# Kernel optimization log

Hardware: AMD Instinct MI355X
Metric: run time of the kernel (lower is better)

## Reference

```python
import jax, jax.numpy as jnp
import numpy as np

EMBED_DIM = 1024
NUM_HEADS = 16
HEAD_DIM = EMBED_DIM // NUM_HEADS
BATCH = 2
SEQ = 2048


def setup_inputs() -> dict:
    key = jax.random.key(0)
    ks = jax.random.split(key, 9)
    s = EMBED_DIM ** -0.5
    inp = {"x": jax.random.normal(ks[0], (BATCH, SEQ, EMBED_DIM), dtype=jnp.float32)}
    names = ["Wq", "Wk", "Wv", "Wo"]
    for i, n in enumerate(names):
        inp[n] = jax.random.normal(ks[1 + i], (EMBED_DIM, EMBED_DIM), dtype=jnp.float32) * s
        inp["b" + n[1]] = jax.random.normal(ks[5 + i], (EMBED_DIM,), dtype=jnp.float32) * 0.02
    return inp


def reference(x, Wq, bq, Wk, bk, Wv, bv, Wo, bo):
    B, S, E = x.shape
    H, D = NUM_HEADS, HEAD_DIM
    scaling = D ** -0.5
    # projections (torch Linear: x @ W.T + b), reshape to (B, H, S, D)
    q = (x @ Wq.T + bq).reshape(B, S, H, D).transpose(0, 2, 1, 3)
    k = (x @ Wk.T + bk).reshape(B, S, H, D).transpose(0, 2, 1, 3)
    v = (x @ Wv.T + bv).reshape(B, S, H, D).transpose(0, 2, 1, 3)
    # full materialized score matrix, matching the original module
    scores = jnp.einsum("bhqd,bhkd->bhqk", q, k) * scaling
    causal = jnp.triu(jnp.ones((S, S), dtype=bool), k=1)  # True above diagonal
    scores = jnp.where(causal[None, None], -jnp.inf, scores)
    attn = jax.nn.softmax(scores, axis=-1)
    out = jnp.einsum("bhqk,bhkd->bhqd", attn, v)  # (B, H, S, D)
    out = out.transpose(0, 2, 1, 3).reshape(B, S, E)
    return out @ Wo.T + bo
```

## Files before the change

kernel.cpp:

```cpp
#include <hip/hip_runtime.h>
#include <stdint.h>

typedef __bf16 bf16;
typedef __bf16 bf16x8 __attribute__((ext_vector_type(8)));
typedef __bf16 bf16x4 __attribute__((ext_vector_type(4)));
typedef float  f32x4  __attribute__((ext_vector_type(4)));

#define E_DIM 1024
#define S_LEN 2048
#define BATCH 2
#define NH 16
#define DH 64

#define NEG_INF (-__builtin_inff())

__device__ __forceinline__ void load_lds16(const bf16* g, bf16* l) {
    __builtin_amdgcn_global_load_lds(
        (const __attribute__((address_space(1))) void*)g,
        (__attribute__((address_space(3))) void*)l, 16, 0, 0);
}

__global__ __launch_bounds__(256) void convert_kernel(
    const float* __restrict__ s0, const float* __restrict__ s1,
    const float* __restrict__ s2, const float* __restrict__ s3,
    const float* __restrict__ s4,
    bf16* __restrict__ d0, bf16* __restrict__ d1, bf16* __restrict__ d2,
    bf16* __restrict__ d3, bf16* __restrict__ d4,
    int n0, int n1)
{
    const float* src; bf16* dst; int n;
    switch (blockIdx.y) {
        case 0:  src = s0; dst = d0; n = n0; break;
        case 1:  src = s1; dst = d1; n = n1; break;
        case 2:  src = s2; dst = d2; n = n1; break;
        case 3:  src = s3; dst = d3; n = n1; break;
        default: src = s4; dst = d4; n = n1; break;
    }
    int i = (blockIdx.x * 256 + threadIdx.x) * 4;
    if (i >= n) return;
    float4 v = *(const float4*)(src + i);
    bf16x4 o;
    o[0] = (bf16)v.x; o[1] = (bf16)v.y; o[2] = (bf16)v.z; o[3] = (bf16)v.w;
    *(bf16x4*)(dst + i) = o;
}

__global__ __launch_bounds__(256) void gemm_kernel(
    const bf16* __restrict__ A,
    const bf16* __restrict__ W0, const bf16* __restrict__ W1, const bf16* __restrict__ W2,
    const float* __restrict__ bias0, const float* __restrict__ bias1, const float* __restrict__ bias2,
    bf16* __restrict__ outQ, bf16* __restrict__ outK, bf16* __restrict__ outVt,
    float* __restrict__ outF, int final_mode)
{
    __shared__ bf16 As[128 * 32];
    __shared__ bf16 Bs[128 * 32];

    int mode;
    const bf16* W; const float* bias;
    if (final_mode) { mode = 3; W = W0; bias = bias0; }
    else {
        mode = blockIdx.z;
        W    = (mode == 0) ? W0 : (mode == 1 ? W1 : W2);
        bias = (mode == 0) ? bias0 : (mode == 1 ? bias1 : bias2);
    }

    const int bm = blockIdx.y * 128, bn = blockIdx.x * 128;
    const int t = threadIdx.x;
    const int lane = t & 63, w = t >> 6;
    const int quad = lane >> 4, l16 = lane & 15;
    const int wm = (w & 1) * 64, wn = (w >> 1) * 64;

    const int r0 = w * 16;
    const int srow = r0 + (lane >> 2), scol = (lane & 3) * 8;
    const bf16* Ag0 = A + (size_t)(bm + srow) * E_DIM + scol;
    const bf16* Ag1 = Ag0 + (size_t)64 * E_DIM;
    const bf16* Wg0 = W + (size_t)(bn + srow) * E_DIM + scol;
    const bf16* Wg1 = Wg0 + (size_t)64 * E_DIM;
    bf16* lda0 = As + r0 * 32;
    bf16* lda1 = As + (64 + r0) * 32;
    bf16* ldb0 = Bs + r0 * 32;
    bf16* ldb1 = Bs + (64 + r0) * 32;

    f32x4 acc[4][4];
#pragma unroll
    for (int i = 0; i < 4; i++)
#pragma unroll
        for (int j = 0; j < 4; j++) acc[i][j] = f32x4{0.f, 0.f, 0.f, 0.f};

    for (int kt = 0; kt < E_DIM; kt += 32) {
        __syncthreads();
        load_lds16(Ag0 + kt, lda0);
        load_lds16(Ag1 + kt, lda1);
        load_lds16(Wg0 + kt, ldb0);
        load_lds16(Wg1 + kt, ldb1);
        __syncthreads();

        bf16x8 af[4], bfr[4];
#pragma unroll
        for (int i = 0; i < 4; i++)
            af[i] = *(const bf16x8*)(As + (wm + i * 16 + l16) * 32 + quad * 8);
#pragma unroll
        for (int j = 0; j < 4; j++)
            bfr[j] = *(const bf16x8*)(Bs + (wn + j * 16 + l16) * 32 + quad * 8);
#pragma unroll
        for (int i = 0; i < 4; i++)
#pragma unroll
            for (int j = 0; j < 4; j++)
                acc[i][j] = __builtin_amdgcn_mfma_f32_16x16x32_bf16(af[i], bfr[j], acc[i][j], 0, 0, 0);
    }

#pragma unroll
    for (int j = 0; j < 4; j++) {
        const int n = bn + wn + j * 16 + l16;
        const float bv = bias[n];
#pragma unroll
        for (int i = 0; i < 4; i++) {
            const int m0 = bm + wm + i * 16 + quad * 4;
            if (mode == 3) {
#pragma unroll
                for (int r = 0; r < 4; r++)
                    outF[(size_t)(m0 + r) * E_DIM + n] = acc[i][j][r] + bv;
            } else if (mode == 2) {
                const int b_ = m0 >> 11, s0 = m0 & (S_LEN - 1);
                const int h = n >> 6, d = n & 63;
                bf16x4 pv;
#pragma unroll
                for (int r = 0; r < 4; r++) pv[r] = (bf16)(acc[i][j][r] + bv);
                *(bf16x4*)(outVt + ((size_t)((b_ * NH + h) * DH + d)) * S_LEN + s0) = pv;
            } else {
                bf16* o = (mode == 0) ? outQ : outK;
                const float sc = (mode == 0) ? 0.125f : 1.0f;
                const int h = n >> 6, d = n & 63;
#pragma unroll
                for (int r = 0; r < 4; r++) {
                    const int m = m0 + r;
                    const int b_ = m >> 11, s = m & (S_LEN - 1);
                    o[((size_t)(b_ * NH + h) * S_LEN + s) * DH + d] = (bf16)((acc[i][j][r] + bv) * sc);
                }
            }
        }
    }
}

__global__ __launch_bounds__(256, 1) void attn_kernel(
    const bf16* __restrict__ Qb, const bf16* __restrict__ Kb,
    const bf16* __restrict__ Vtb, bf16* __restrict__ Ob)
{
    __shared__ bf16 Ks[128 * 72];
    __shared__ bf16 Vs[64 * 136];
    __shared__ bf16 Ps[4][16 * 136];

    const int t = threadIdx.x, lane = t & 63, w = t >> 6;
    const int quad = lane >> 4, l16 = lane & 15;

    const int i = blockIdx.x;
    const int xcd = i & 7, rr = i >> 3;
    const int bh = (xcd << 2) | (rr & 3);
    const int pr = rr >> 2;
    const int qlo = pr, qhi = 15 - pr;

    const bf16* Qg = Qb + (size_t)bh * S_LEN * DH;
    const bf16* Kg = Kb + (size_t)bh * S_LEN * DH;
    const bf16* Vg = Vtb + (size_t)bh * DH * S_LEN;
    const int b_ = bh >> 4, h = bh & 15;
    bf16* Og = Ob + (size_t)b_ * S_LEN * E_DIM + h * DH;

    bf16* Pw = Ps[w];
    const int inrow0 = w * 32;

    bf16x8 aq[2][2][2];
#pragma unroll
    for (int qt = 0; qt < 2; qt++) {
        const int qrow0 = (qt ? qhi : qlo) * 128 + inrow0;
#pragma unroll
        for (int st = 0; st < 2; st++) {
            const bf16* qp = Qg + (size_t)(qrow0 + st * 16 + l16) * DH + quad * 8;
            aq[qt][st][0] = *(const bf16x8*)(qp);
            aq[qt][st][1] = *(const bf16x8*)(qp + 32);
        }
    }

    f32x4 o[2][2][4];
    float l_part[2][2][4];
#pragma unroll
    for (int qt = 0; qt < 2; qt++)
#pragma unroll
        for (int st = 0; st < 2; st++)
#pragma unroll
            for (int dt = 0; dt < 4; dt++) {
                o[qt][st][dt] = f32x4{0.f, 0.f, 0.f, 0.f};
                l_part[qt][st][dt] = 0.f;
            }

    const int T = qhi + 1;
    const int krow = t >> 3, kcol8 = (t & 7) * 8;
    const int vrow = t >> 4, vcol8 = (t & 15) * 8;

    uint4 kc[4], vc[4];
#pragma unroll
    for (int k = 0; k < 4; k++)
        kc[k] = *(const uint4*)(Kg + (size_t)(krow + 32 * k) * DH + kcol8);
#pragma unroll
    for (int k = 0; k < 4; k++)
        vc[k] = *(const uint4*)(Vg + (size_t)(vrow + 16 * k) * S_LEN + vcol8);

    for (int kt = 0; kt < T; kt++) {
        __syncthreads();
#pragma unroll
        for (int k = 0; k < 4; k++)
            *(uint4*)(Ks + (krow + 32 * k) * 72 + kcol8) = kc[k];
#pragma unroll
        for (int k = 0; k < 4; k++)
            *(uint4*)(Vs + (vrow + 16 * k) * 136 + vcol8) = vc[k];
        __syncthreads();

        if (kt + 1 < T) {
            const int nb = (kt + 1) * 128;
#pragma unroll
            for (int k = 0; k < 4; k++)
                kc[k] = *(const uint4*)(Kg + (size_t)(nb + krow + 32 * k) * DH + kcol8);
#pragma unroll
            for (int k = 0; k < 4; k++)
                vc[k] = *(const uint4*)(Vg + (size_t)(vrow + 16 * k) * S_LEN + nb + vcol8);
        }

#pragma unroll
        for (int qt = 0; qt < 2; qt++) {
            if (qt == 0 && kt > qlo) continue;
            const bool diag = qt ? (kt == qhi) : (kt == qlo);

#pragma unroll
            for (int st = 0; st < 2; st++) {
                const int inrow_base = inrow0 + st * 16 + quad * 4;

                f32x4 sv[8];
#pragma unroll
                for (int jt = 0; jt < 8; jt++) {
                    const bf16* kp = Ks + (jt * 16 + l16) * 72 + quad * 8;
                    bf16x8 bk0 = *(const bf16x8*)(kp);
                    bf16x8 bk1 = *(const bf16x8*)(kp + 32);
                    f32x4 s = f32x4{0.f, 0.f, 0.f, 0.f};
                    s = __builtin_amdgcn_mfma_f32_16x16x32_bf16(aq[qt][st][0], bk0, s, 0, 0, 0);
                    s = __builtin_amdgcn_mfma_f32_16x16x32_bf16(aq[qt][st][1], bk1, s, 0, 0, 0);
                    sv[jt] = s;
                }

                if (diag) {
#pragma unroll
                    for (int jt = 0; jt < 8; jt++) {
                        const int kcol = jt * 16 + l16;
#pragma unroll
                        for (int r = 0; r < 4; r++)
                            if (kcol > inrow_base + r) sv[jt][r] = NEG_INF;
                    }
                }

#pragma unroll
                for (int jt = 0; jt < 8; jt++)
#pragma unroll
                    for (int r = 0; r < 4; r++) {
                        const float pe = __expf(sv[jt][r]);
                        sv[jt][r] = pe;
                        l_part[qt][st][r] += pe;
                    }

#pragma unroll
                for (int jt = 0; jt < 8; jt++)
#pragma unroll
                    for (int r = 0; r < 4; r++)
                        Pw[(quad * 4 + r) * 136 + jt * 16 + l16] = (bf16)sv[jt][r];

#pragma unroll
                for (int ks = 0; ks < 4; ks++) {
                    bf16x8 ap = *(const bf16x8*)(Pw + l16 * 136 + ks * 32 + quad * 8);
#pragma unroll
                    for (int dt = 0; dt < 4; dt++) {
                        bf16x8 bv = *(const bf16x8*)(Vs + (dt * 16 + l16) * 136 + ks * 32 + quad * 8);
                        o[qt][st][dt] = __builtin_amdgcn_mfma_f32_16x16x32_bf16(ap, bv, o[qt][st][dt], 0, 0, 0);
                    }
                }
            }
        }
    }

#pragma unroll
    for (int qt = 0; qt < 2; qt++) {
        const int qrow0 = (qt ? qhi : qlo) * 128 + inrow0;
#pragma unroll
        for (int st = 0; st < 2; st++) {
#pragma unroll
            for (int r = 0; r < 4; r++) {
                float l = l_part[qt][st][r];
                l += __shfl_xor(l, 1);
                l += __shfl_xor(l, 2);
                l += __shfl_xor(l, 4);
                l += __shfl_xor(l, 8);
                l_part[qt][st][r] = 1.0f / l;
            }
#pragma unroll
            for (int r = 0; r < 4; r++) {
                const int srow = qrow0 + st * 16 + quad * 4 + r;
#pragma unroll
                for (int dt = 0; dt < 4; dt++)
                    Og[(size_t)srow * E_DIM + dt * 16 + l16] =
                        (bf16)(o[qt][st][dt][r] * l_part[qt][st][r]);
            }
        }
    }
}

extern "C" void kernel_launch(void* const* d_in, const int* in_sizes, int n_in,
                              void* d_out, int out_size, void* d_ws, size_t ws_size,
                              hipStream_t stream)
{
    const float* x  = (const float*)d_in[0];
    const float* Wq = (const float*)d_in[1];
    const float* bq = (const float*)d_in[2];
    const float* Wk = (const float*)d_in[3];
    const float* bk = (const float*)d_in[4];
    const float* Wv = (const float*)d_in[5];
    const float* bv = (const float*)d_in[6];
    const float* Wo = (const float*)d_in[7];
    const float* bo = (const float*)d_in[8];
    float* out = (float*)d_out;

    char* ws = (char*)d_ws;
    const size_t MB = 1ull << 20;
    bf16* xb  = (bf16*)(ws + 0);
    bf16* wqb = (bf16*)(ws + 8 * MB);
    bf16* wkb = (bf16*)(ws + 10 * MB);
    bf16* wvb = (bf16*)(ws + 12 * MB);
    bf16* wob = (bf16*)(ws + 14 * MB);
    bf16* Qb  = (bf16*)(ws + 16 * MB);
    bf16* Kb  = (bf16*)(ws + 24 * MB);
    bf16* Vtb = (bf16*)(ws + 32 * MB);
    bf16* Ab  = (bf16*)(ws + 40 * MB);

    convert_kernel<<<dim3(4096, 5), 256, 0, stream>>>(
        x, Wq, Wk, Wv, Wo, xb, wqb, wkb, wvb, wob, 4194304, 1048576);

    gemm_kernel<<<dim3(8, 32, 3), 256, 0, stream>>>(
        xb, wqb, wkb, wvb, bq, bk, bv, Qb, Kb, Vtb, nullptr, 0);

    attn_kernel<<<dim3(256), 256, 0, stream>>>(Qb, Kb, Vtb, Ab);

    gemm_kernel<<<dim3(8, 32, 1), 256, 0, stream>>>(
        Ab, wob, wob, wob, bo, bo, bo, nullptr, nullptr, nullptr, out, 1);
}
```

Measured before the change: 233.0 us.

## Deepen GEMM K-step to 64 and share K/V fragments across attention subtiles

```diff
diff --git a/kernel.cpp b/kernel.cpp
--- a/kernel.cpp
+++ b/kernel.cpp
@@ -51,8 +51,8 @@
     bf16* __restrict__ outQ, bf16* __restrict__ outK, bf16* __restrict__ outVt,
     float* __restrict__ outF, int final_mode)
 {
-    __shared__ bf16 As[128 * 32];
-    __shared__ bf16 Bs[128 * 32];
+    __shared__ bf16 As0[128 * 32], As1[128 * 32];
+    __shared__ bf16 Bs0[128 * 32], Bs1[128 * 32];
 
     int mode;
     const bf16* W; const float* bias;
@@ -75,10 +75,10 @@
     const bf16* Ag1 = Ag0 + (size_t)64 * E_DIM;
     const bf16* Wg0 = W + (size_t)(bn + srow) * E_DIM + scol;
     const bf16* Wg1 = Wg0 + (size_t)64 * E_DIM;
-    bf16* lda0 = As + r0 * 32;
-    bf16* lda1 = As + (64 + r0) * 32;
-    bf16* ldb0 = Bs + r0 * 32;
-    bf16* ldb1 = Bs + (64 + r0) * 32;
+    bf16* a00 = As0 + r0 * 32;  bf16* a01 = As0 + (64 + r0) * 32;
+    bf16* a10 = As1 + r0 * 32;  bf16* a11 = As1 + (64 + r0) * 32;
+    bf16* b00 = Bs0 + r0 * 32;  bf16* b01 = Bs0 + (64 + r0) * 32;
+    bf16* b10 = Bs1 + r0 * 32;  bf16* b11 = Bs1 + (64 + r0) * 32;
 
     f32x4 acc[4][4];
 #pragma unroll
@@ -86,26 +86,35 @@
 #pragma unroll
         for (int j = 0; j < 4; j++) acc[i][j] = f32x4{0.f, 0.f, 0.f, 0.f};
 
-    for (int kt = 0; kt < E_DIM; kt += 32) {
+    for (int kt = 0; kt < E_DIM; kt += 64) {
         __syncthreads();
-        load_lds16(Ag0 + kt, lda0);
-        load_lds16(Ag1 + kt, lda1);
-        load_lds16(Wg0 + kt, ldb0);
-        load_lds16(Wg1 + kt, ldb1);
+        load_lds16(Ag0 + kt,      a00);
+        load_lds16(Ag1 + kt,      a01);
+        load_lds16(Ag0 + kt + 32, a10);
+        load_lds16(Ag1 + kt + 32, a11);
+        load_lds16(Wg0 + kt,      b00);
+        load_lds16(Wg1 + kt,      b01);
+        load_lds16(Wg0 + kt + 32, b10);
+        load_lds16(Wg1 + kt + 32, b11);
         __syncthreads();
 
-        bf16x8 af[4], bfr[4];
-#pragma unroll
-        for (int i = 0; i < 4; i++)
-            af[i] = *(const bf16x8*)(As + (wm + i * 16 + l16) * 32 + quad * 8);
-#pragma unroll
-        for (int j = 0; j < 4; j++)
-            bfr[j] = *(const bf16x8*)(Bs + (wn + j * 16 + l16) * 32 + quad * 8);
-#pragma unroll
-        for (int i = 0; i < 4; i++)
+#pragma unroll
+        for (int half = 0; half < 2; half++) {
+            const bf16* Asx = half ? As1 : As0;
+            const bf16* Bsx = half ? Bs1 : Bs0;
+            bf16x8 af[4], bfr[4];
+#pragma unroll
+            for (int i = 0; i < 4; i++)
+                af[i] = *(const bf16x8*)(Asx + (wm + i * 16 + l16) * 32 + quad * 8);
 #pragma unroll
             for (int j = 0; j < 4; j++)
-                acc[i][j] = __builtin_amdgcn_mfma_f32_16x16x32_bf16(af[i], bfr[j], acc[i][j], 0, 0, 0);
+                bfr[j] = *(const bf16x8*)(Bsx + (wn + j * 16 + l16) * 32 + quad * 8);
+#pragma unroll
+            for (int i = 0; i < 4; i++)
+#pragma unroll
+                for (int j = 0; j < 4; j++)
+                    acc[i][j] = __builtin_amdgcn_mfma_f32_16x16x32_bf16(af[i], bfr[j], acc[i][j], 0, 0, 0);
+        }
     }
 
 #pragma unroll
@@ -147,7 +156,7 @@
 {
     __shared__ bf16 Ks[128 * 72];
     __shared__ bf16 Vs[64 * 136];
-    __shared__ bf16 Ps[4][16 * 136];
+    __shared__ bf16 Ps[4][32 * 136];
 
     const int t = threadIdx.x, lane = t & 63, w = t >> 6;
     const int quad = lane >> 4, l16 = lane & 15;
@@ -228,55 +237,63 @@
             if (qt == 0 && kt > qlo) continue;
             const bool diag = qt ? (kt == qhi) : (kt == qlo);
 
-#pragma unroll
-            for (int st = 0; st < 2; st++) {
-                const int inrow_base = inrow0 + st * 16 + quad * 4;
-
-                f32x4 sv[8];
-#pragma unroll
-                for (int jt = 0; jt < 8; jt++) {
-                    const bf16* kp = Ks + (jt * 16 + l16) * 72 + quad * 8;
-                    bf16x8 bk0 = *(const bf16x8*)(kp);
-                    bf16x8 bk1 = *(const bf16x8*)(kp + 32);
+            f32x4 sv[2][8];
+#pragma unroll
+            for (int jt = 0; jt < 8; jt++) {
+                const bf16* kp = Ks + (jt * 16 + l16) * 72 + quad * 8;
+                bf16x8 bk0 = *(const bf16x8*)(kp);
+                bf16x8 bk1 = *(const bf16x8*)(kp + 32);
+#pragma unroll
+                for (int st = 0; st < 2; st++) {
                     f32x4 s = f32x4{0.f, 0.f, 0.f, 0.f};
                     s = __builtin_amdgcn_mfma_f32_16x16x32_bf16(aq[qt][st][0], bk0, s, 0, 0, 0);
                     s = __builtin_amdgcn_mfma_f32_16x16x32_bf16(aq[qt][st][1], bk1, s, 0, 0, 0);
-                    sv[jt] = s;
+                    sv[st][jt] = s;
                 }
-
-                if (diag) {
+            }
+
+            if (diag) {
+#pragma unroll
+                for (int st = 0; st < 2; st++) {
+                    const int inrow_base = inrow0 + st * 16 + quad * 4;
 #pragma unroll
                     for (int jt = 0; jt < 8; jt++) {
                         const int kcol = jt * 16 + l16;
 #pragma unroll
                         for (int r = 0; r < 4; r++)
-                            if (kcol > inrow_base + r) sv[jt][r] = NEG_INF;
+                            if (kcol > inrow_base + r) sv[st][jt][r] = NEG_INF;
                     }
                 }
-
+            }
+
+#pragma unroll
+            for (int st = 0; st < 2; st++)
 #pragma unroll
                 for (int jt = 0; jt < 8; jt++)
 #pragma unroll
                     for (int r = 0; r < 4; r++) {
-                        const float pe = __expf(sv[jt][r]);
-                        sv[jt][r] = pe;
+                        const float pe = __expf(sv[st][jt][r]);
+                        sv[st][jt][r] = pe;
                         l_part[qt][st][r] += pe;
                     }
 
 #pragma unroll
+            for (int st = 0; st < 2; st++)
+#pragma unroll
                 for (int jt = 0; jt < 8; jt++)
 #pragma unroll
                     for (int r = 0; r < 4; r++)
-                        Pw[(quad * 4 + r) * 136 + jt * 16 + l16] = (bf16)sv[jt][r];
-
-#pragma unroll
-                for (int ks = 0; ks < 4; ks++) {
-                    bf16x8 ap = *(const bf16x8*)(Pw + l16 * 136 + ks * 32 + quad * 8);
-#pragma unroll
-                    for (int dt = 0; dt < 4; dt++) {
-                        bf16x8 bv = *(const bf16x8*)(Vs + (dt * 16 + l16) * 136 + ks * 32 + quad * 8);
-                        o[qt][st][dt] = __builtin_amdgcn_mfma_f32_16x16x32_bf16(ap, bv, o[qt][st][dt], 0, 0, 0);
-                    }
+                        Pw[(st * 16 + quad * 4 + r) * 136 + jt * 16 + l16] = (bf16)sv[st][jt][r];
+
+#pragma unroll
+            for (int ks = 0; ks < 4; ks++) {
+                bf16x8 ap0 = *(const bf16x8*)(Pw + l16 * 136 + ks * 32 + quad * 8);
+                bf16x8 ap1 = *(const bf16x8*)(Pw + (16 + l16) * 136 + ks * 32 + quad * 8);
+#pragma unroll
+                for (int dt = 0; dt < 4; dt++) {
+                    bf16x8 bv = *(const bf16x8*)(Vs + (dt * 16 + l16) * 136 + ks * 32 + quad * 8);
+                    o[qt][0][dt] = __builtin_amdgcn_mfma_f32_16x16x32_bf16(ap0, bv, o[qt][0][dt], 0, 0, 0);
+                    o[qt][1][dt] = __builtin_amdgcn_mfma_f32_16x16x32_bf16(ap1, bv, o[qt][1][dt], 0, 0, 0);
                 }
             }
         }
```

Result: no change. 237.6 us (+2.0%).
